# Kernel optimization log

Hardware: AMD Instinct MI355X
Metric: run time of the kernel (lower is better)

## Reference

```python
import jax, jax.numpy as jnp
import numpy as np

B, L, S, D, H, NS, NSLOT = 2, 2048, 2048, 1024, 16, 8, 512
HD = D // H


def _silu(x):
    return x * jax.nn.sigmoid(x)


def _layernorm(x, g, b, eps=1e-5):
    mu = jnp.mean(x, axis=-1, keepdims=True)
    var = jnp.var(x, axis=-1, keepdims=True)
    return (x - mu) * jax.lax.rsqrt(var + eps) * g + b


def setup_inputs() -> dict:
    key = jax.random.key(0)
    ks = jax.random.split(key, 12)
    x_q = jax.random.normal(ks[0], (B, L, D), dtype=jnp.float32)
    x_idx = jax.random.randint(ks[1], (B, S), 0, NSLOT)
    E_slots = jax.random.normal(ks[2], (NSLOT, D), dtype=jnp.float32)
    # EMA decay rates close to 1 so multi-scale gates stay non-degenerate over S steps
    rhos = 1.0 - 0.005 * jax.random.uniform(ks[3], (NS,), dtype=jnp.float32)
    C_seq = jax.random.uniform(ks[4], (B, L, NS), dtype=jnp.float32)
    s = 1.0 / np.sqrt(D)
    Wq = jax.random.normal(ks[5], (D, D), dtype=jnp.float32) * s
    Wk = jax.random.normal(ks[6], (D, D), dtype=jnp.float32) * s
    Wv = jax.random.normal(ks[7], (D, D), dtype=jnp.float32) * s
    Wo = jax.random.normal(ks[8], (D, D), dtype=jnp.float32) * s
    Wpe = jax.random.normal(ks[9], (D, NS), dtype=jnp.float32) * (1.0 / np.sqrt(NS))
    ln_kv_g = jnp.ones((D,), jnp.float32); ln_kv_b = jnp.zeros((D,), jnp.float32)
    ln_q_g = jnp.ones((D,), jnp.float32); ln_q_b = jnp.zeros((D,), jnp.float32)
    return dict(x_q=x_q, x_idx=x_idx, E_slots=E_slots, rhos=rhos, C_seq=C_seq,
                Wq=Wq, Wk=Wk, Wv=Wv, Wo=Wo, Wpe=Wpe,
                ln_kv_g=ln_kv_g, ln_kv_b=ln_kv_b, ln_q_g=ln_q_g, ln_q_b=ln_q_b)


def reference(x_q, x_idx, E_slots, rhos, C_seq, Wq, Wk, Wv, Wo, Wpe,
              ln_kv_g, ln_kv_b, ln_q_g, ln_q_b):
    # --- KV side: memory = ln_kv(E_slots); K/V = proj(memory); gather by slot id ---
    mem = _layernorm(E_slots, ln_kv_g, ln_kv_b)          # [NSLOT, D]
    Ek = mem @ Wk.T                                       # [NSLOT, D]
    Ev = mem @ Wv.T
    K = Ek[x_idx]                                         # [B, S, D] embedding lookup
    V = Ev[x_idx]
    # --- multiplicative EMA gate per kv position: c[s,m] = rho_m^(age) ---
    ages = (S - 1 - jnp.arange(S)).astype(x_q.dtype)      # [S]
    c_kv = jnp.power(rhos[None, :], ages[:, None])        # [S, NS]
    gate_kv = _silu(c_kv @ Wpe.T)                         # [S, D] = SiLU(pe_proj(C))
    K = K * gate_kv[None]
    V = V * gate_kv[None]
    # --- symmetric query gating: Q = q_proj(ln_q(x_q * SiLU(pe_proj(C_seq)))) ---
    gate_q = _silu(C_seq @ Wpe.T)                         # [B, L, D]
    Q = _layernorm(x_q * gate_q, ln_q_g, ln_q_b) @ Wq.T   # [B, L, D]
    # --- multi-head softmax attention ---
    q = Q.reshape(B, L, H, HD)
    k = K.reshape(B, S, H, HD)
    v = V.reshape(B, S, H, HD)
    scores = jnp.einsum('blhd,bshd->bhls', q, k) / np.sqrt(HD).astype(np.float32)
    attn = jax.nn.softmax(scores, axis=-1)                # [B, H, L, S]
    out = jnp.einsum('bhls,bshd->blhd', attn, v).reshape(B, L, D)
    return out @ Wo.T                                     # o_proj (dropout = identity, eval)
```

## Files before the change

kernel.cpp:

```cpp
#include <hip/hip_runtime.h>
#include <cmath>
#include <cstddef>

namespace {

constexpr int cB = 2, cL = 2048, cS = 2048, cD = 1024, cH = 16, cNS = 8, cNSLOT = 512, cHD = 64;

typedef __attribute__((ext_vector_type(8))) short short8;
typedef __attribute__((ext_vector_type(4))) float f32x4;

#define MFMA16(a, b, c) __builtin_amdgcn_mfma_f32_16x16x32_bf16((a), (b), (c), 0, 0, 0)

__device__ __forceinline__ float sigmoidf_(float x) { return 1.f / (1.f + __expf(-x)); }

__device__ __forceinline__ unsigned short f2bf(float x) {
  union { float f; unsigned u; } c; c.f = x;
  unsigned r = c.u + 0x7FFFu + ((c.u >> 16) & 1u);
  return (unsigned short)(r >> 16);
}
__device__ __forceinline__ float bf2f(unsigned short h) {
  union { unsigned u; float f; } c; c.u = ((unsigned)h) << 16;
  return c.f;
}

__device__ __forceinline__ void unpack8(const uint4 a, const uint4 b, short8& p0, short8& p1) {
  const unsigned p[8] = {a.x, a.y, a.z, a.w, b.x, b.y, b.z, b.w};
  union { unsigned u[4]; short8 s; } H, L;
#pragma unroll
  for (int i = 0; i < 4; i++) {
    H.u[i] = __builtin_amdgcn_perm(p[2 * i + 1], p[2 * i], 0x05040100u);
    L.u[i] = __builtin_amdgcn_perm(p[2 * i + 1], p[2 * i], 0x07060302u);
  }
  p0 = H.s;
  p1 = L.s;
}

__device__ __forceinline__ void async16(const void* g, void* l) {
  __builtin_amdgcn_global_load_lds((const __attribute__((address_space(1))) void*)g,
                                   (__attribute__((address_space(3))) void*)l, 16, 0, 0);
}

__global__ __launch_bounds__(256) void prep_all_kernel(
    const float* __restrict__ Wq, const float* __restrict__ Wk,
    const float* __restrict__ Wv, const float* __restrict__ Wo,
    unsigned short* __restrict__ Wqh, unsigned short* __restrict__ Wql,
    unsigned short* __restrict__ Wkh, unsigned short* __restrict__ Wkl,
    unsigned short* __restrict__ Wvh, unsigned short* __restrict__ Wvl,
    unsigned short* __restrict__ Woh, unsigned short* __restrict__ Wol,
    const float* __restrict__ E, const float* __restrict__ lnkv_g,
    const float* __restrict__ lnkv_b, unsigned short* __restrict__ mh,
    const float* __restrict__ rhos,
    const float* __restrict__ Wpe, float* __restrict__ gkv,
    const float* __restrict__ xq, const float* __restrict__ Cseq,
    const float* __restrict__ lnq_g, const float* __restrict__ lnq_b,
    unsigned short* __restrict__ Yh) {
  __shared__ float sC[cNS];
  __shared__ float rbuf[8];
  const int bid = blockIdx.x;
  const int tid = threadIdx.x;

  if (bid < 2048) {
    const int wid = bid >> 9;
    const size_t off = ((size_t)(bid & 511) * 256 + tid) * 8;
    const float* src = wid == 0 ? Wq : wid == 1 ? Wk : wid == 2 ? Wv : Wo;
    unsigned short* dh = wid == 0 ? Wqh : wid == 1 ? Wkh : wid == 2 ? Wvh : Woh;
    unsigned short* dl = wid == 0 ? Wql : wid == 1 ? Wkl : wid == 2 ? Wvl : Wol;
    const float4 a = *(const float4*)(src + off);
    const float4 b = *(const float4*)(src + off + 4);
    float v[8] = {a.x, a.y, a.z, a.w, b.x, b.y, b.z, b.w};
    unsigned short h8[8], l8[8];
#pragma unroll
    for (int j = 0; j < 8; j++) {
      h8[j] = f2bf(v[j]);
      l8[j] = f2bf(v[j] - bf2f(h8[j]));
    }
    *(uint4*)(dh + off) = *(uint4*)h8;
    *(uint4*)(dl + off) = *(uint4*)l8;
  } else if (bid < 2560) {
    const int row = bid - 2048;
    const int d0 = tid * 4;
    const float4 x = *(const float4*)(E + (size_t)row * cD + d0);
    float s1 = x.x + x.y + x.z + x.w;
    float s2 = x.x * x.x + x.y * x.y + x.z * x.z + x.w * x.w;
#pragma unroll
    for (int o = 32; o > 0; o >>= 1) { s1 += __shfl_xor(s1, o, 64); s2 += __shfl_xor(s2, o, 64); }
    if ((tid & 63) == 0) { rbuf[tid >> 6] = s1; rbuf[4 + (tid >> 6)] = s2; }
    __syncthreads();
    s1 = rbuf[0] + rbuf[1] + rbuf[2] + rbuf[3];
    s2 = rbuf[4] + rbuf[5] + rbuf[6] + rbuf[7];
    const float mean = s1 * (1.f / cD);
    const float var = s2 * (1.f / cD) - mean * mean;
    const float inv = rsqrtf(var + 1e-5f);
    const float4 g = *(const float4*)(lnkv_g + d0);
    const float4 b = *(const float4*)(lnkv_b + d0);
    unsigned short h4[4];
    h4[0] = f2bf((x.x - mean) * inv * g.x + b.x);
    h4[1] = f2bf((x.y - mean) * inv * g.y + b.y);
    h4[2] = f2bf((x.z - mean) * inv * g.z + b.z);
    h4[3] = f2bf((x.w - mean) * inv * g.w + b.w);
    *(uint2*)(mh + (size_t)row * cD + d0) = *(uint2*)h4;
  } else if (bid < 4608) {
    const int s = bid - 2560;
    if (tid < cNS) {
      const float age = (float)(cS - 1 - s);
      sC[tid] = __expf(age * __logf(rhos[tid]));
    }
    __syncthreads();
    const int d0 = tid * 4;
    float4 o4;
#pragma unroll
    for (int j = 0; j < 4; j++) {
      const float* wr = Wpe + (size_t)(d0 + j) * cNS;
      float gs = 0.f;
#pragma unroll
      for (int m = 0; m < cNS; m++) gs += sC[m] * wr[m];
      ((float*)&o4)[j] = gs * sigmoidf_(gs);
    }
    *(float4*)(gkv + (size_t)s * cD + d0) = o4;
  } else {
    const int row = bid - 4608;
    if (tid < cNS) sC[tid] = Cseq[(size_t)row * cNS + tid];
    __syncthreads();
    const int d0 = tid * 4;
    const float4 x = *(const float4*)(xq + (size_t)row * cD + d0);
    float y[4];
    float s1 = 0.f, s2 = 0.f;
#pragma unroll
    for (int j = 0; j < 4; j++) {
      const float* wr = Wpe + (size_t)(d0 + j) * cNS;
      float gs = 0.f;
#pragma unroll
      for (int m = 0; m < cNS; m++) gs += sC[m] * wr[m];
      const float val = ((const float*)&x)[j] * gs * sigmoidf_(gs);
      y[j] = val;
      s1 += val;
      s2 += val * val;
    }
#pragma unroll
    for (int o = 32; o > 0; o >>= 1) { s1 += __shfl_xor(s1, o, 64); s2 += __shfl_xor(s2, o, 64); }
    if ((tid & 63) == 0) { rbuf[tid >> 6] = s1; rbuf[4 + (tid >> 6)] = s2; }
    __syncthreads();
    s1 = rbuf[0] + rbuf[1] + rbuf[2] + rbuf[3];
    s2 = rbuf[4] + rbuf[5] + rbuf[6] + rbuf[7];
    const float mean = s1 * (1.f / cD);
    const float var = s2 * (1.f / cD) - mean * mean;
    const float inv = rsqrtf(var + 1e-5f);
    const float4 g = *(const float4*)(lnq_g + d0);
    const float4 b = *(const float4*)(lnq_b + d0);
    unsigned short h4[4];
    h4[0] = f2bf((y[0] - mean) * inv * g.x + b.x);
    h4[1] = f2bf((y[1] - mean) * inv * g.y + b.y);
    h4[2] = f2bf((y[2] - mean) * inv * g.z + b.z);
    h4[3] = f2bf((y[3] - mean) * inv * g.w + b.w);
    *(uint2*)(Yh + (size_t)row * cD + d0) = *(uint2*)h4;
  }
}

template <int MODE>
__device__ __forceinline__ void gemm2_body(
    const unsigned short* __restrict__ Ahi,
    const unsigned short* __restrict__ Whi, const unsigned short* __restrict__ Wlo,
    float* __restrict__ Cf, unsigned short* __restrict__ Chi,
    int m0, int n0, int N, int K, float scale,
    unsigned short* sA, unsigned short* sBh, unsigned short* sBl) {
  const int tid = threadIdx.x;
  const int wave = tid >> 6, lane = tid & 63;
  const int quad = lane >> 4, l16 = lane & 15;
  const int wy = wave >> 1, wx = wave & 1;
  const int sg = (lane & 3) ^ ((lane >> 3) & 3);
  const int srow = lane >> 2;
  (void)srow;

  f32x4 acc[4][2];
#pragma unroll
  for (int i = 0; i < 4; i++)
#pragma unroll
    for (int j = 0; j < 2; j++) acc[i][j] = (f32x4){0.f, 0.f, 0.f, 0.f};

  auto stage = [&](int buf, int k0) {
#pragma unroll
    for (int c = 0; c < 2; c++) {
      const int row = c * 64 + wave * 16 + (lane >> 2);
      const size_t ga = (size_t)(m0 + row) * K + k0 + sg * 8;
      async16(Ahi + ga, sA + buf * 4096 + (c * 64 + wave * 16) * 32);
    }
    const int rowb = wave * 16 + (lane >> 2);
    const size_t gb = (size_t)(n0 + rowb) * K + k0 + sg * 8;
    async16(Whi + gb, sBh + buf * 2048 + wave * 16 * 32);
    async16(Wlo + gb, sBl + buf * 2048 + wave * 16 * 32);
  };

  stage(0, 0);
  __syncthreads();
  const int aswz = (l16 >> 1) & 3;
  int buf = 0;
  for (int k0 = 0; k0 < K; k0 += 32, buf ^= 1) {
    if (k0 + 32 < K) stage(buf ^ 1, k0 + 32);
    short8 bh[2], bl2[2];
#pragma unroll
    for (int tj = 0; tj < 2; tj++) {
      const int br = (wx * 32 + tj * 16 + l16) * 32 + ((quad ^ aswz) * 8);
      bh[tj] = *(const short8*)(sBh + buf * 2048 + br);
      bl2[tj] = *(const short8*)(sBl + buf * 2048 + br);
    }
#pragma unroll
    for (int ti = 0; ti < 4; ti++) {
      const int ar = (wy * 64 + ti * 16 + l16) * 32 + ((quad ^ aswz) * 8);
      const short8 ah = *(const short8*)(sA + buf * 4096 + ar);
#pragma unroll
      for (int tj = 0; tj < 2; tj++) {
        acc[ti][tj] = MFMA16(ah, bh[tj], acc[ti][tj]);
        acc[ti][tj] = MFMA16(ah, bl2[tj], acc[ti][tj]);
      }
    }
    __syncthreads();
  }

#pragma unroll
  for (int ti = 0; ti < 4; ti++)
#pragma unroll
    for (int tj = 0; tj < 2; tj++) {
      const int row = m0 + wy * 64 + ti * 16 + quad * 4;
      const int col = n0 + wx * 32 + tj * 16 + l16;
#pragma unroll
      for (int r = 0; r < 4; r++) {
        const size_t idx = (size_t)(row + r) * N + col;
        if constexpr (MODE == 0) {
          Cf[idx] = acc[ti][tj][r];
        } else {
          Chi[idx] = f2bf(acc[ti][tj][r] * scale);
        }
      }
    }
}

__global__ __launch_bounds__(256, 3) void gemm_qkv_kernel(
    const unsigned short* __restrict__ memhi,
    const unsigned short* __restrict__ Wkhi, const unsigned short* __restrict__ Wklo,
    const unsigned short* __restrict__ Wvhi, const unsigned short* __restrict__ Wvlo,
    float* __restrict__ Ek, float* __restrict__ Ev,
    const unsigned short* __restrict__ Yhi,
    const unsigned short* __restrict__ Wqhi, const unsigned short* __restrict__ Wqlo,
    unsigned short* __restrict__ qhi, float qscale) {
  __shared__ __align__(16) unsigned short sA[2 * 128 * 32];
  __shared__ __align__(16) unsigned short sBh[2 * 64 * 32];
  __shared__ __align__(16) unsigned short sBl[2 * 64 * 32];
  const int bid = blockIdx.x;
  if (bid < 128) {
    const int z = bid >> 6, rem = bid & 63;
    const int m0 = (rem >> 4) * 128, n0 = (rem & 15) * 64;
    gemm2_body<0>(memhi, z ? Wvhi : Wkhi, z ? Wvlo : Wklo, z ? Ev : Ek, nullptr,
                  m0, n0, cD, cD, 1.f, sA, sBh, sBl);
  } else {
    const int lid = bid - 128;
    const int m0 = (lid >> 4) * 128, n0 = (lid & 15) * 64;
    gemm2_body<1>(Yhi, Wqhi, Wqlo, nullptr, qhi, m0, n0, cD, cD, qscale, sA, sBh, sBl);
  }
}

__global__ __launch_bounds__(256, 3) void gemm_o_kernel(
    const unsigned short* __restrict__ AOhi,
    const unsigned short* __restrict__ Wohi, const unsigned short* __restrict__ Wolo,
    float* __restrict__ out) {
  __shared__ __align__(16) unsigned short sA[2 * 128 * 32];
  __shared__ __align__(16) unsigned short sBh[2 * 64 * 32];
  __shared__ __align__(16) unsigned short sBl[2 * 64 * 32];
  gemm2_body<0>(AOhi, Wohi, Wolo, out, nullptr, blockIdx.y * 128, blockIdx.x * 64,
                cD, cD, 1.f, sA, sBh, sBl);
}

__global__ __launch_bounds__(256) void prep_kv_kernel(
    const float* __restrict__ Ek, const float* __restrict__ Ev,
    const float* __restrict__ gkv, const int* __restrict__ xidx,
    unsigned short* __restrict__ Khi, unsigned short* __restrict__ Vthi) {
  __shared__ float tile[64][65];
  const int bid = blockIdx.x;
  const int tid = threadIdx.x;
  if (bid < 2048) {
    const int t = bid * 256 + tid;
    const int d0 = (t & 127) * 8;
    const int s = (t >> 7) & (cS - 1);
    const int b = t >> 18;
    const int slot = xidx[b * cS + s];
    const float4 e0 = *(const float4*)(Ek + (size_t)slot * cD + d0);
    const float4 e1 = *(const float4*)(Ek + (size_t)slot * cD + d0 + 4);
    const float4 g0 = *(const float4*)(gkv + (size_t)s * cD + d0);
    const float4 g1 = *(const float4*)(gkv + (size_t)s * cD + d0 + 4);
    float v[8] = {e0.x * g0.x, e0.y * g0.y, e0.z * g0.z, e0.w * g0.w,
                  e1.x * g1.x, e1.y * g1.y, e1.z * g1.z, e1.w * g1.w};
    unsigned short h8[8];
#pragma unroll
    for (int j = 0; j < 8; j++) h8[j] = f2bf(v[j]);
    *(uint4*)(Khi + (size_t)(b * cS + s) * cD + d0) = *(uint4*)h8;
  } else {
    const int local = bid - 2048;
    const int s0 = (local & 31) * 64;
    const int d0 = ((local >> 5) & 15) * 64;
    const int b = local >> 9;
    const int sl = tid >> 4;
    const int dl = (tid & 15) * 4;
#pragma unroll
    for (int it = 0; it < 4; it++) {
      const int s = s0 + sl + it * 16;
      const int slot = xidx[b * cS + s];
      const float4 e = *(const float4*)(Ev + (size_t)slot * cD + d0 + dl);
      const float4 g = *(const float4*)(gkv + (size_t)s * cD + d0 + dl);
      tile[sl + it * 16][dl + 0] = e.x * g.x;
      tile[sl + it * 16][dl + 1] = e.y * g.y;
      tile[sl + it * 16][dl + 2] = e.z * g.z;
      tile[sl + it * 16][dl + 3] = e.w * g.w;
    }
    __syncthreads();
    const int dr = tid >> 3;
    const int sc = (tid & 7) * 8;
#pragma unroll
    for (int it = 0; it < 2; it++) {
      const int d = d0 + dr + it * 32;
      unsigned short h8[8];
#pragma unroll
      for (int j = 0; j < 8; j++) h8[j] = f2bf(tile[sc + j][dr + it * 32]);
      *(uint4*)(Vthi + (size_t)(b * cD + d) * cS + s0 + sc) = *(uint4*)h8;
    }
  }
}

__global__ __launch_bounds__(128, 3) void attn_mfma_kernel(
    const unsigned short* __restrict__ qhi,
    const unsigned short* __restrict__ Khi,
    const unsigned short* __restrict__ Vthi,
    unsigned short* __restrict__ AOhi) {
  __shared__ __align__(16) unsigned short sKh[64 * 64];
  __shared__ __align__(16) unsigned short sVh[64 * 64];
  __shared__ __align__(16) unsigned int sP32[2][16][68];

  const int tid = threadIdx.x;
  const int wave = tid >> 6, lane = tid & 63;
  const int quad = lane >> 4, l16 = lane & 15;
  const int lB = blockIdx.x * 64;
  const int h = blockIdx.y, b = blockIdx.z;

  short8 qh[2][2];
#pragma unroll
  for (int t = 0; t < 2; t++) {
    const size_t base =
        (size_t)(b * cL + lB + wave * 32 + t * 16 + l16) * cD + h * cHD + quad * 8;
    qh[t][0] = *(const short8*)(qhi + base);
    qh[t][1] = *(const short8*)(qhi + base + 32);
  }

  short8 ones;
#pragma unroll
  for (int i = 0; i < 8; i++) ones[i] = (short)0x3F80;

  f32x4 O[2][4], dacc[2];
#pragma unroll
  for (int t = 0; t < 2; t++) {
#pragma unroll
    for (int i = 0; i < 4; i++) O[t][i] = (f32x4){0.f, 0.f, 0.f, 0.f};
    dacc[t] = (f32x4){0.f, 0.f, 0.f, 0.f};
  }

  const int srow8 = lane >> 3;
  const int sg = (lane & 7) ^ srow8;

  const int r0 = (wave * 4 + 0) * 8 + srow8;
  const int r1 = (wave * 4 + 1) * 8 + srow8;
  const int r2 = (wave * 4 + 2) * 8 + srow8;
  const int r3 = (wave * 4 + 3) * 8 + srow8;
  const size_t kb0 = (size_t)(b * cS + r0) * cD + h * cHD + sg * 8;
  const size_t kb1 = (size_t)(b * cS + r1) * cD + h * cHD + sg * 8;
  const size_t kb2 = (size_t)(b * cS + r2) * cD + h * cHD + sg * 8;
  const size_t kb3 = (size_t)(b * cS + r3) * cD + h * cHD + sg * 8;
  const size_t vb0 = (size_t)(b * cD + h * cHD + r0) * cS + sg * 8;
  const size_t vb1 = (size_t)(b * cD + h * cHD + r1) * cS + sg * 8;
  const size_t vb2 = (size_t)(b * cD + h * cHD + r2) * cS + sg * 8;
  const size_t vb3 = (size_t)(b * cD + h * cHD + r3) * cS + sg * 8;

  uint4 k0, k1, k2, k3, v0, v1, v2, v3;
  k0 = *(const uint4*)(Khi + kb0);
  k1 = *(const uint4*)(Khi + kb1);
  k2 = *(const uint4*)(Khi + kb2);
  k3 = *(const uint4*)(Khi + kb3);
  v0 = *(const uint4*)(Vthi + vb0);
  v1 = *(const uint4*)(Vthi + vb1);
  v2 = *(const uint4*)(Vthi + vb2);
  v3 = *(const uint4*)(Vthi + vb3);

  const int j0 = wave * 4;

  for (int s0 = 0; s0 < cS; s0 += 64) {
    __syncthreads();
    *(uint4*)&sKh[(j0 + 0) * 512 + lane * 8] = k0;
    *(uint4*)&sKh[(j0 + 1) * 512 + lane * 8] = k1;
    *(uint4*)&sKh[(j0 + 2) * 512 + lane * 8] = k2;
    *(uint4*)&sKh[(j0 + 3) * 512 + lane * 8] = k3;
    *(uint4*)&sVh[(j0 + 0) * 512 + lane * 8] = v0;
    *(uint4*)&sVh[(j0 + 1) * 512 + lane * 8] = v1;
    *(uint4*)&sVh[(j0 + 2) * 512 + lane * 8] = v2;
    *(uint4*)&sVh[(j0 + 3) * 512 + lane * 8] = v3;
    __syncthreads();

    {
      const int sn = (s0 + 64) & (cS - 1);
      const size_t kc = (size_t)sn * cD;
      k0 = *(const uint4*)(Khi + kb0 + kc);
      k1 = *(const uint4*)(Khi + kb1 + kc);
      k2 = *(const uint4*)(Khi + kb2 + kc);
      k3 = *(const uint4*)(Khi + kb3 + kc);
      v0 = *(const uint4*)(Vthi + vb0 + sn);
      v1 = *(const uint4*)(Vthi + vb1 + sn);
      v2 = *(const uint4*)(Vthi + vb2 + sn);
      v3 = *(const uint4*)(Vthi + vb3 + sn);
    }

    f32x4 sc[2][4];
#pragma unroll
    for (int t = 0; t < 2; t++)
#pragma unroll
      for (int st = 0; st < 4; st++) sc[t][st] = (f32x4){0.f, 0.f, 0.f, 0.f};
#pragma unroll
    for (int st = 0; st < 4; st++) {
      const int srw = st * 16 + l16;
#pragma unroll
      for (int ks = 0; ks < 2; ks++) {
        const int slot = (ks * 4 + quad) ^ (srw & 7);
        const short8 kfh = *(const short8*)&sKh[srw * 64 + slot * 8];
        sc[0][st] = MFMA16(qh[0][ks], kfh, sc[0][st]);
        sc[1][st] = MFMA16(qh[1][ks], kfh, sc[1][st]);
      }
    }

#pragma unroll
    for (int st = 0; st < 4; st++)
#pragma unroll
      for (int r = 0; r < 4; r++) {
        const unsigned u0 = f2bf(__builtin_amdgcn_exp2f(sc[0][st][r]));
        const unsigned u1 = f2bf(__builtin_amdgcn_exp2f(sc[1][st][r]));
        sP32[wave][quad * 4 + r][st * 16 + l16] = (u1 << 16) | u0;
      }

    short8 pf0[2], pf1[2];
#pragma unroll
    for (int ss = 0; ss < 2; ss++) {
      const uint4 pa = *(const uint4*)&sP32[wave][l16][ss * 32 + quad * 8];
      const uint4 pb = *(const uint4*)&sP32[wave][l16][ss * 32 + quad * 8 + 4];
      unpack8(pa, pb, pf0[ss], pf1[ss]);
    }

#pragma unroll
    for (int dt = 0; dt < 4; dt++) {
      const int drw = dt * 16 + l16;
#pragma unroll
      for (int ss = 0; ss < 2; ss++) {
        const int slot = (ss * 4 + quad) ^ (drw & 7);
        const short8 vfh = *(const short8*)&sVh[drw * 64 + slot * 8];
        O[0][dt] = MFMA16(pf0[ss], vfh, O[0][dt]);
        O[1][dt] = MFMA16(pf1[ss], vfh, O[1][dt]);
      }
    }
    dacc[0] = MFMA16(pf0[0], ones, dacc[0]);
    dacc[0] = MFMA16(pf0[1], ones, dacc[0]);
    dacc[1] = MFMA16(pf1[0], ones, dacc[1]);
    dacc[1] = MFMA16(pf1[1], ones, dacc[1]);
  }

#pragma unroll
  for (int t = 0; t < 2; t++) {
    float inv[4];
#pragma unroll
    for (int r = 0; r < 4; r++) inv[r] = 1.f / dacc[t][r];
#pragma unroll
    for (int dt = 0; dt < 4; dt++)
#pragma unroll
      for (int r = 0; r < 4; r++) {
        const size_t l = (size_t)(b * cL + lB + wave * 32 + t * 16 + quad * 4 + r);
        AOhi[l * cD + h * cHD + dt * 16 + l16] = f2bf(O[t][dt][r] * inv[r]);
      }
  }
}

}

extern "C" void kernel_launch(void* const* d_in, const int* in_sizes, int n_in,
                              void* d_out, int out_size, void* d_ws, size_t ws_size,
                              hipStream_t stream) {
  (void)in_sizes; (void)n_in; (void)out_size; (void)ws_size;
  const float* x_q = (const float*)d_in[0];
  const int* x_idx = (const int*)d_in[1];
  const float* E_slots = (const float*)d_in[2];
  const float* rhos = (const float*)d_in[3];
  const float* C_seq = (const float*)d_in[4];
  const float* Wq = (const float*)d_in[5];
  const float* Wk = (const float*)d_in[6];
  const float* Wv = (const float*)d_in[7];
  const float* Wo = (const float*)d_in[8];
  const float* Wpe = (const float*)d_in[9];
  const float* ln_kv_g = (const float*)d_in[10];
  const float* ln_kv_b = (const float*)d_in[11];
  const float* ln_q_g = (const float*)d_in[12];
  const float* ln_q_b = (const float*)d_in[13];
  float* out = (float*)d_out;

  float* ws = (float*)d_ws;
  unsigned short* memhi = (unsigned short*)(ws + 0);
  unsigned short* Wkhi = (unsigned short*)(ws + 262144);
  unsigned short* Wklo = (unsigned short*)(ws + 786432);
  unsigned short* Wvhi = (unsigned short*)(ws + 1310720);
  unsigned short* Wvlo = (unsigned short*)(ws + 1835008);
  float* gkv = ws + 2359296;
  unsigned short* Wqhi = (unsigned short*)(ws + 4456448);
  unsigned short* Wqlo = (unsigned short*)(ws + 4980736);
  unsigned short* Wohi = (unsigned short*)(ws + 5505024);
  unsigned short* Wolo = (unsigned short*)(ws + 6029312);
  float* Ek = ws + 6553600;
  float* Ev = ws + 7077888;
  unsigned short* Yhi = (unsigned short*)(ws + 7602176);
  unsigned short* AOhi = (unsigned short*)(ws + 7602176);
  unsigned short* qhi = (unsigned short*)(ws + 9699328);
  unsigned short* Khi = (unsigned short*)(ws + 11796480);
  unsigned short* Vthi = (unsigned short*)(ws + 13893632);

  constexpr float kQScale = 0.125f * 1.44269504088896340736f;

  prep_all_kernel<<<8704, 256, 0, stream>>>(
      Wq, Wk, Wv, Wo, Wqhi, Wqlo, Wkhi, Wklo, Wvhi, Wvlo, Wohi, Wolo,
      E_slots, ln_kv_g, ln_kv_b, memhi, rhos, Wpe, gkv,
      x_q, C_seq, ln_q_g, ln_q_b, Yhi);
  gemm_qkv_kernel<<<640, 256, 0, stream>>>(
      memhi, Wkhi, Wklo, Wvhi, Wvlo, Ek, Ev, Yhi, Wqhi, Wqlo, qhi, kQScale);
  prep_kv_kernel<<<3072, 256, 0, stream>>>(Ek, Ev, gkv, x_idx, Khi, Vthi);
  attn_mfma_kernel<<<dim3(cL / 64, cH, cB), 128, 0, stream>>>(qhi, Khi, Vthi, AOhi);
  gemm_o_kernel<<<dim3(16, 32), 256, 0, stream>>>(AOhi, Wohi, Wolo, out);
}
```

Baseline: 260.0 us.

## Split attention over two key halves with atomic fp32 accumulation and normalize pass

The attention grid doubles by splitting the S dimension into two halves, one block per half. Each block atomically adds its unnormalized output and softmax denominator into fp32 workspace buffers. A zero-fill kernel runs before attention and a normalization kernel after it, which divides and converts to bf16. This is meant to improve CU occupancy and tail balance, since the old grid of 1024 blocks did not fill the GPU evenly. The cost is two extra launches, a large volume of atomic traffic and extra fp32 round trips; the bf16 packing of probabilities also switches to a single packed convert instruction.

```diff
diff --git a/kernel.cpp b/kernel.cpp
--- a/kernel.cpp
+++ b/kernel.cpp
@@ -324,11 +324,20 @@
   }
 }
 
+__global__ __launch_bounds__(256) void zero_acc_kernel(float* __restrict__ p) {
+  const size_t off = (size_t)blockIdx.x * 4096 + (size_t)threadIdx.x * 16;
+  const float4 z = {0.f, 0.f, 0.f, 0.f};
+  *(float4*)(p + off) = z;
+  *(float4*)(p + off + 4) = z;
+  *(float4*)(p + off + 8) = z;
+  *(float4*)(p + off + 12) = z;
+}
+
 __global__ __launch_bounds__(128, 3) void attn_mfma_kernel(
     const unsigned short* __restrict__ qhi,
     const unsigned short* __restrict__ Khi,
     const unsigned short* __restrict__ Vthi,
-    unsigned short* __restrict__ AOhi) {
+    float* __restrict__ Oacc, float* __restrict__ Dacc) {
   __shared__ __align__(16) unsigned short sKh[64 * 64];
   __shared__ __align__(16) unsigned short sVh[64 * 64];
   __shared__ __align__(16) unsigned int sP32[2][16][68];
@@ -337,7 +346,10 @@
   const int wave = tid >> 6, lane = tid & 63;
   const int quad = lane >> 4, l16 = lane & 15;
   const int lB = blockIdx.x * 64;
-  const int h = blockIdx.y, b = blockIdx.z;
+  const int h = blockIdx.y;
+  const int zb = blockIdx.z;
+  const int b = zb >> 1, sp = zb & 1;
+  const int sbeg = sp * (cS / 2);
 
   short8 qh[2][2];
 #pragma unroll
@@ -377,18 +389,21 @@
   const size_t vb3 = (size_t)(b * cD + h * cHD + r3) * cS + sg * 8;
 
   uint4 k0, k1, k2, k3, v0, v1, v2, v3;
-  k0 = *(const uint4*)(Khi + kb0);
-  k1 = *(const uint4*)(Khi + kb1);
-  k2 = *(const uint4*)(Khi + kb2);
-  k3 = *(const uint4*)(Khi + kb3);
-  v0 = *(const uint4*)(Vthi + vb0);
-  v1 = *(const uint4*)(Vthi + vb1);
-  v2 = *(const uint4*)(Vthi + vb2);
-  v3 = *(const uint4*)(Vthi + vb3);
+  {
+    const size_t kc0 = (size_t)sbeg * cD;
+    k0 = *(const uint4*)(Khi + kb0 + kc0);
+    k1 = *(const uint4*)(Khi + kb1 + kc0);
+    k2 = *(const uint4*)(Khi + kb2 + kc0);
+    k3 = *(const uint4*)(Khi + kb3 + kc0);
+    v0 = *(const uint4*)(Vthi + vb0 + sbeg);
+    v1 = *(const uint4*)(Vthi + vb1 + sbeg);
+    v2 = *(const uint4*)(Vthi + vb2 + sbeg);
+    v3 = *(const uint4*)(Vthi + vb3 + sbeg);
+  }
 
   const int j0 = wave * 4;
 
-  for (int s0 = 0; s0 < cS; s0 += 64) {
+  for (int s0 = sbeg; s0 < sbeg + cS / 2; s0 += 64) {
     __syncthreads();
     *(uint4*)&sKh[(j0 + 0) * 512 + lane * 8] = k0;
     *(uint4*)&sKh[(j0 + 1) * 512 + lane * 8] = k1;
@@ -401,7 +416,7 @@
     __syncthreads();
 
     {
-      const int sn = (s0 + 64) & (cS - 1);
+      const int sn = sbeg + ((s0 + 64) & (cS / 2 - 1));
       const size_t kc = (size_t)sn * cD;
       k0 = *(const uint4*)(Khi + kb0 + kc);
       k1 = *(const uint4*)(Khi + kb1 + kc);
@@ -434,9 +449,11 @@
     for (int st = 0; st < 4; st++)
 #pragma unroll
       for (int r = 0; r < 4; r++) {
-        const unsigned u0 = f2bf(__builtin_amdgcn_exp2f(sc[0][st][r]));
-        const unsigned u1 = f2bf(__builtin_amdgcn_exp2f(sc[1][st][r]));
-        sP32[wave][quad * 4 + r][st * 16 + l16] = (u1 << 16) | u0;
+        const float e0 = __builtin_amdgcn_exp2f(sc[0][st][r]);
+        const float e1 = __builtin_amdgcn_exp2f(sc[1][st][r]);
+        unsigned pk;
+        asm("v_cvt_pk_bf16_f32 %0, %1, %2" : "=v"(pk) : "v"(e0), "v"(e1));
+        sP32[wave][quad * 4 + r][st * 16 + l16] = pk;
       }
 
     short8 pf0[2], pf1[2];
@@ -466,17 +483,37 @@
 
 #pragma unroll
   for (int t = 0; t < 2; t++) {
-    float inv[4];
-#pragma unroll
-    for (int r = 0; r < 4; r++) inv[r] = 1.f / dacc[t][r];
 #pragma unroll
     for (int dt = 0; dt < 4; dt++)
 #pragma unroll
       for (int r = 0; r < 4; r++) {
         const size_t l = (size_t)(b * cL + lB + wave * 32 + t * 16 + quad * 4 + r);
-        AOhi[l * cD + h * cHD + dt * 16 + l16] = f2bf(O[t][dt][r] * inv[r]);
-      }
-  }
+        atomicAdd(&Oacc[l * cD + h * cHD + dt * 16 + l16], O[t][dt][r]);
+      }
+    if (l16 == 0) {
+#pragma unroll
+      for (int r = 0; r < 4; r++) {
+        const size_t l = (size_t)(b * cL + lB + wave * 32 + t * 16 + quad * 4 + r);
+        atomicAdd(&Dacc[l * cH + h], dacc[t][r]);
+      }
+    }
+  }
+}
+
+__global__ __launch_bounds__(256) void attn_norm_kernel(
+    const float* __restrict__ Oacc, const float* __restrict__ Dacc,
+    unsigned short* __restrict__ AOhi) {
+  const int row = blockIdx.x;
+  const int d0 = threadIdx.x * 4;
+  const int h = d0 >> 6;
+  const float inv = 1.f / Dacc[(size_t)row * cH + h];
+  const float4 o = *(const float4*)(Oacc + (size_t)row * cD + d0);
+  unsigned short h4[4];
+  h4[0] = f2bf(o.x * inv);
+  h4[1] = f2bf(o.y * inv);
+  h4[2] = f2bf(o.z * inv);
+  h4[3] = f2bf(o.w * inv);
+  *(uint2*)(AOhi + (size_t)row * cD + d0) = *(uint2*)h4;
 }
 
 }
@@ -519,6 +556,8 @@
   unsigned short* qhi = (unsigned short*)(ws + 9699328);
   unsigned short* Khi = (unsigned short*)(ws + 11796480);
   unsigned short* Vthi = (unsigned short*)(ws + 13893632);
+  float* Oacc = ws + 0;
+  float* Dacc = ws + 4194304;
 
   constexpr float kQScale = 0.125f * 1.44269504088896340736f;
 
@@ -529,6 +568,8 @@
   gemm_qkv_kernel<<<640, 256, 0, stream>>>(
       memhi, Wkhi, Wklo, Wvhi, Wvlo, Ek, Ev, Yhi, Wqhi, Wqlo, qhi, kQScale);
   prep_kv_kernel<<<3072, 256, 0, stream>>>(Ek, Ev, gkv, x_idx, Khi, Vthi);
-  attn_mfma_kernel<<<dim3(cL / 64, cH, cB), 128, 0, stream>>>(qhi, Khi, Vthi, AOhi);
+  zero_acc_kernel<<<1040, 256, 0, stream>>>(ws);
+  attn_mfma_kernel<<<dim3(cL / 64, cH, cB * 2), 128, 0, stream>>>(qhi, Khi, Vthi, Oacc, Dacc);
+  attn_norm_kernel<<<cB * cL, 256, 0, stream>>>(Oacc, Dacc, AOhi);
   gemm_o_kernel<<<dim3(16, 32), 256, 0, stream>>>(AOhi, Wohi, Wolo, out);
 }
```

Result: slower. 277.2 us (+6.6%).
